# Performance work log

Hardware: AMD Instinct MI355X
Metric: run time of the kernel (lower is better)

Reference implementation:

```python
import jax, jax.numpy as jnp
import numpy as np

HID = 256
HEADS = 8
HD = HID // HEADS  # head_dim = 32


def setup_inputs() -> dict:
    key = jax.random.key(0)
    ks = jax.random.split(key, 16)
    B, N = 4, 2048
    s = 0.02
    inp = {
        'x': jax.random.normal(ks[0], (B, N, 4, HID), dtype=jnp.float32),
        'Wq': jax.random.normal(ks[1], (HID, HID), dtype=jnp.float32) * s,
        'bq': jnp.zeros((HID,), jnp.float32),
        'Wk': jax.random.normal(ks[2], (HID, HID), dtype=jnp.float32) * s,
        'bk': jnp.zeros((HID,), jnp.float32),
        'Wv': jax.random.normal(ks[3], (HID, HID), dtype=jnp.float32) * s,
        'bv': jnp.zeros((HID,), jnp.float32),
        'Wvec': jax.random.normal(ks[4], (2 * HID, HID), dtype=jnp.float32) * s,
        'Wo': jax.random.normal(ks[5], (3 * HID, HID), dtype=jnp.float32) * s,
        'bo': jnp.zeros((3 * HID,), jnp.float32),
        'Wg': jax.random.normal(ks[6], (HID, 2 * HID), dtype=jnp.float32) * s,
        'bg': jnp.zeros((HID,), jnp.float32),
        'alpha_dot': jnp.asarray(1.0, jnp.float32),
        'alpha_norm': jnp.asarray(1.0, jnp.float32),
    }
    return inp


def reference(x, Wq, bq, Wk, bk, Wv, bv, Wvec, Wo, bo, Wg, bg, alpha_dot, alpha_norm):
    B, N, _, H = x.shape
    nh, hd = HEADS, HD
    x_scalar = x[:, :, 0]          # (B,N,H)
    vec = x[:, :, 1:]              # (B,N,3,H)

    def lin(a, W, b=None):
        y = a @ W.T
        return y + b if b is not None else y

    # scalar q/k/v -> (B,heads,N,hd)
    q = lin(x_scalar, Wq, bq).reshape(B, N, nh, hd).transpose(0, 2, 1, 3)
    k = lin(x_scalar, Wk, bk).reshape(B, N, nh, hd).transpose(0, 2, 1, 3)
    v = lin(x_scalar, Wv, bv).reshape(B, N, nh, hd).transpose(0, 2, 1, 3)

    # invariant features from vector channels
    vec_proj = lin(vec, Wvec)                  # (B,N,3,2H)
    vec1, vec2 = vec_proj[..., :H], vec_proj[..., H:]
    vec_dot = jnp.sum(vec1 * vec2, axis=-2)    # (B,N,H)
    vec_norm = jnp.linalg.norm(vec, axis=2)    # (B,N,H)

    # equivariant values: (B,heads,N,3*hd)
    vec_v = vec.reshape(B, N, 3, nh, hd).transpose(0, 3, 1, 2, 4).reshape(B, nh, N, 3 * hd)

    # fused attention: one softmax, aggregate scalar v and vector v together
    scale = 1.0 / np.sqrt(hd).astype(np.float32)
    scores = jnp.einsum('bhqd,bhkd->bhqk', q, k) * scale
    attn = jax.nn.softmax(scores, axis=-1)
    v_all = jnp.concatenate([v, vec_v], axis=-1)        # (B,h,N,4*hd)
    out_all = jnp.einsum('bhqk,bhkd->bhqd', attn, v_all)
    out_s, out_v = out_all[..., :hd], out_all[..., hd:]

    x_out = out_s.transpose(0, 2, 1, 3).reshape(B, N, H)
    vec_aggr = out_v.reshape(B, nh, N, 3, hd).transpose(0, 2, 3, 1, 4).reshape(B, N, 3, H)

    invariants = jnp.concatenate([alpha_dot * vec_dot, alpha_norm * vec_norm], axis=-1)
    gate = jax.nn.sigmoid(lin(invariants, Wg, bg))[:, :, None, :]  # (B,N,1,H)
    vec_combined = gate * vec_aggr + vec  # vector_mixing='add', gating=True

    o = lin(x_out, Wo, bo)
    o1, o2, o3 = o[..., :H], o[..., H:2 * H], o[..., 2 * H:]
    x_updated = vec_dot * o1 + vec_norm * o2 + o3

    x_final = jnp.concatenate([x_updated[:, :, None, :], vec_combined], axis=2)  # (B,N,4,H)
    return x_final
```

## Files before the change

kernel.cpp:

```cpp
#include <hip/hip_runtime.h>
#include <cstdint>
#include <cstddef>

#define HIDN 256
#define NHEAD 8
#define HD 32
#define NSEQ 2048
#define QS (0.17677669529663687f * 1.4426950408889634f)

typedef __attribute__((ext_vector_type(8))) short short8;
typedef __attribute__((ext_vector_type(4))) short short4v;
typedef __attribute__((ext_vector_type(4))) float f32x4;
typedef __attribute__((ext_vector_type(16))) float f32x16;
typedef __attribute__((ext_vector_type(4))) uint32_t u32x4;

static __device__ __forceinline__ short f2bf(float f) {
    union { float f; uint32_t u; } v; v.f = f;
    uint32_t r = (v.u + 0x7FFF + ((v.u >> 16) & 1)) >> 16;
    return (short)r;
}
static __device__ __forceinline__ float bf2f(short s) {
    union { uint32_t u; float f; } v; v.u = ((uint32_t)(uint16_t)s) << 16;
    return v.f;
}

static __device__ __forceinline__ float ex2(float x) {
#if defined(__has_builtin)
#if __has_builtin(__builtin_amdgcn_exp2f)
    return __builtin_amdgcn_exp2f(x);
#else
    return exp2f(x);
#endif
#else
    return exp2f(x);
#endif
}

static __device__ __forceinline__ uint32_t pkbf16(float lo, float hi) {
    uint32_t r;
    asm("v_cvt_pk_bf16_f32 %0, %1, %2" : "=v"(r) : "v"(lo), "v"(hi));
    return r;
}

static __device__ __forceinline__ void half_bcast(uint32_t x, uint32_t& lo, uint32_t& hi) {
    uint32_t a = x, b = x;
    asm("v_permlane32_swap_b32 %0, %1" : "+v"(a), "+v"(b));
    lo = a; hi = b;
}

static __device__ __forceinline__ void gload16(const void* g, void* l) {
    __builtin_amdgcn_global_load_lds(
        (__attribute__((address_space(1))) void*)g,
        (__attribute__((address_space(3))) void*)l, 16, 0, 0);
}

static __device__ __forceinline__ f32x16 zero16() {
    f32x16 z;
    #pragma unroll
    for (int i = 0; i < 16; i++) z[i] = 0.f;
    return z;
}

__global__ __launch_bounds__(256) void wcvt_kernel(
    const float* __restrict__ Wq, const float* __restrict__ Wk,
    const float* __restrict__ Wv, const float* __restrict__ Wvec,
    const float* __restrict__ Wo, const float* __restrict__ Wg,
    const float* __restrict__ bq, const float* __restrict__ bk,
    const float* __restrict__ bv,
    const float* __restrict__ ad, const float* __restrict__ an,
    short* __restrict__ Wqkvb, short* __restrict__ Wvecb,
    short* __restrict__ Wob, short* __restrict__ Wgb, float* __restrict__ bqkvs)
{
    int idx = blockIdx.x * 256 + threadIdx.x;
    if (idx < 65536)        Wqkvb[idx] = f2bf(Wq[idx] * QS);
    else if (idx < 131072)  Wqkvb[idx] = f2bf(Wk[idx - 65536]);
    else if (idx < 196608)  Wqkvb[idx] = f2bf(Wv[idx - 131072]);
    else if (idx < 327680)  Wvecb[idx - 196608] = f2bf(Wvec[idx - 196608]);
    else if (idx < 524288)  Wob[idx - 327680] = f2bf(Wo[idx - 327680]);
    else {
        int i2 = idx - 524288;
        int k = i2 & 511;
        float s = (k < 256) ? ad[0] : an[0];
        Wgb[i2] = f2bf(Wg[i2] * s);
    }
    if (idx < 256)          bqkvs[idx] = bq[idx] * QS;
    else if (idx < 512)     bqkvs[idx] = bk[idx - 256];
    else if (idx < 768)     bqkvs[idx] = bv[idx - 512];
}

__global__ __launch_bounds__(256) void qkv_kernel(
    const float* __restrict__ x, const short* __restrict__ Wqkvb,
    const float* __restrict__ bqkvs,
    short* __restrict__ qbf, short* __restrict__ kbf, short* __restrict__ vtb)
{
    __shared__ short xs[32 * 264];
    __shared__ short vtmp[256 * 34];
    const int tid = threadIdx.x;
    const int m0 = blockIdx.x * 32;
    const int b  = m0 >> 11;
    const int n0 = m0 & 2047;

    #pragma unroll
    for (int l = 0; l < 8; l++) {
        int i = l * 256 + tid;
        int t = i >> 6, j4 = i & 63;
        float4 v = *(const float4*)(x + (size_t)(m0 + t) * 1024 + j4 * 4);
        short4v s = { f2bf(v.x), f2bf(v.y), f2bf(v.z), f2bf(v.w) };
        *(short4v*)&xs[t * 264 + j4 * 4] = s;
    }
    __syncthreads();

    const int wave = tid >> 6, lane = tid & 63;
    const int col = lane & 15, quad = lane >> 4;

    short8 xf[2][8];
    #pragma unroll
    for (int mt = 0; mt < 2; mt++)
        #pragma unroll
        for (int kk = 0; kk < 8; kk++)
            xf[mt][kk] = *(const short8*)&xs[(mt * 16 + col) * 264 + kk * 32 + quad * 8];

    #pragma unroll
    for (int y = 0; y < 3; y++) {
        f32x4 acc[2][4];
        #pragma unroll
        for (int mt = 0; mt < 2; mt++)
            #pragma unroll
            for (int nt = 0; nt < 4; nt++) acc[mt][nt] = (f32x4){0.f,0.f,0.f,0.f};

        const short* Wb = Wqkvb + (size_t)(y * 256 + wave * 64) * 256;
        #pragma unroll
        for (int kk = 0; kk < 8; kk++) {
            #pragma unroll
            for (int nt = 0; nt < 4; nt++) {
                short8 wf = *(const short8*)(Wb + (size_t)(nt * 16 + col) * 256 + kk * 32 + quad * 8);
                #pragma unroll
                for (int mt = 0; mt < 2; mt++)
                    acc[mt][nt] = __builtin_amdgcn_mfma_f32_16x16x32_bf16(wf, xf[mt][kk], acc[mt][nt], 0, 0, 0);
            }
        }

        if (y == 0) {
            #pragma unroll
            for (int nt = 0; nt < 4; nt++) {
                int ch = wave * 64 + nt * 16 + quad * 4;
                float4 bi = *(const float4*)&bqkvs[ch];
                int h = ch >> 5, d = ch & 31;
                #pragma unroll
                for (int mt = 0; mt < 2; mt++) {
                    int n = n0 + mt * 16 + col;
                    short4v s = { f2bf(acc[mt][nt][0] + bi.x), f2bf(acc[mt][nt][1] + bi.y),
                                  f2bf(acc[mt][nt][2] + bi.z), f2bf(acc[mt][nt][3] + bi.w) };
                    *(short4v*)(qbf + ((size_t)(b * 8 + h) * 2048 + n) * 32 + d) = s;
                }
            }
        } else if (y == 1) {
            #pragma unroll
            for (int nt = 0; nt < 4; nt++) {
                int ch = wave * 64 + nt * 16 + quad * 4;
                float4 bi = *(const float4*)&bqkvs[256 + ch];
                int h = ch >> 5, d = ch & 31;
                #pragma unroll
                for (int mt = 0; mt < 2; mt++) {
                    int n = n0 + mt * 16 + col;
                    short4v s = { f2bf(acc[mt][nt][0] + bi.x), f2bf(acc[mt][nt][1] + bi.y),
                                  f2bf(acc[mt][nt][2] + bi.z), f2bf(acc[mt][nt][3] + bi.w) };
                    int f  = ((n & 63) >> 5) * 2 + (d >> 4);
                    int lk = (n & 31) + (((d >> 3) & 1) << 5);
                    short* dst = kbf + ((size_t)(b * 8 + h) * 32 + (n >> 6)) * 2048
                               + f * 512 + lk * 8 + (d & 7);
                    *(short4v*)dst = s;
                }
            }
        } else {
            #pragma unroll
            for (int nt = 0; nt < 4; nt++) {
                int ch = wave * 64 + nt * 16 + quad * 4;
                float4 bi = *(const float4*)&bqkvs[512 + ch];
                #pragma unroll
                for (int mt = 0; mt < 2; mt++) {
                    int tok = mt * 16 + col;
                    vtmp[(ch + 0) * 34 + tok] = f2bf(acc[mt][nt][0] + bi.x);
                    vtmp[(ch + 1) * 34 + tok] = f2bf(acc[mt][nt][1] + bi.y);
                    vtmp[(ch + 2) * 34 + tok] = f2bf(acc[mt][nt][2] + bi.z);
                    vtmp[(ch + 3) * 34 + tok] = f2bf(acc[mt][nt][3] + bi.w);
                }
            }
        }
    }
    __syncthreads();
    {
        int ch = tid;
        short s[32];
        #pragma unroll
        for (int t = 0; t < 32; t++) s[t] = vtmp[ch * 34 + t];
        int h = ch >> 5, d = ch & 31;
        size_t tile = (size_t)(b * 8 + h) * 32 + (n0 >> 6);
        short* dst = vtb + tile * 8192;
        #pragma unroll
        for (int g = 0; g < 4; g++) {
            int kbse = (n0 & 63) + g * 8;
            int f = kbse >> 4;
            int h2 = (kbse >> 3) & 1;
            *(short8*)(dst + f * 512 + (d + h2 * 32) * 8) = *(short8*)&s[g * 8];
        }
    }
}

__global__ __launch_bounds__(512) void vec_kernel(
    const float* __restrict__ x, const short* __restrict__ Wvecb,
    float* __restrict__ dotb, short* __restrict__ invb,
    float* __restrict__ normb, short* __restrict__ vtb)
{
    __shared__ short vb[3 * 16 * 264];
    const int tid = threadIdx.x;
    const int m0 = blockIdx.x * 16;
    const int b = m0 >> 11, n0 = m0 & 2047;

    #pragma unroll
    for (int p = 0; p < 6; p++) {
        int f4 = p * 512 + tid;
        int t = f4 / 192;
        int rem = f4 - t * 192;
        int c = rem >> 6, j4 = rem & 63;
        float4 v = *(const float4*)(x + (size_t)(m0 + t) * 1024 + 256 + c * 256 + j4 * 4);
        short4v s = { f2bf(v.x), f2bf(v.y), f2bf(v.z), f2bf(v.w) };
        *(short4v*)&vb[(c * 16 + t) * 264 + j4 * 4] = s;
    }
    __syncthreads();

    const int wave = tid >> 6, lane = tid & 63;
    const int col = lane & 15, quad = lane >> 4;
    const int j0 = wave * 32;

    f32x4 d1[3][2], d2[3][2];
    #pragma unroll
    for (int c = 0; c < 3; c++)
        #pragma unroll
        for (int nt = 0; nt < 2; nt++) {
            d1[c][nt] = (f32x4){0.f,0.f,0.f,0.f};
            d2[c][nt] = (f32x4){0.f,0.f,0.f,0.f};
        }

    #pragma unroll
    for (int kk = 0; kk < 8; kk++) {
        short8 w1[2], w2[2];
        #pragma unroll
        for (int nt = 0; nt < 2; nt++) {
            w1[nt] = *(const short8*)&Wvecb[(size_t)(j0 + nt * 16 + col) * 256 + kk * 32 + quad * 8];
            w2[nt] = *(const short8*)&Wvecb[(size_t)(256 + j0 + nt * 16 + col) * 256 + kk * 32 + quad * 8];
        }
        #pragma unroll
        for (int c = 0; c < 3; c++) {
            short8 xf = *(const short8*)&vb[(c * 16 + col) * 264 + kk * 32 + quad * 8];
            #pragma unroll
            for (int nt = 0; nt < 2; nt++) {
                d1[c][nt] = __builtin_amdgcn_mfma_f32_16x16x32_bf16(w1[nt], xf, d1[c][nt], 0, 0, 0);
                d2[c][nt] = __builtin_amdgcn_mfma_f32_16x16x32_bf16(w2[nt], xf, d2[c][nt], 0, 0, 0);
            }
        }
    }
    #pragma unroll
    for (int nt = 0; nt < 2; nt++) {
        f32x4 dac = d1[0][nt] * d2[0][nt] + d1[1][nt] * d2[1][nt] + d1[2][nt] * d2[2][nt];
        float4 o = { dac[0], dac[1], dac[2], dac[3] };
        *(float4*)&dotb[(size_t)(m0 + col) * 256 + j0 + nt * 16 + quad * 4] = o;
        short4v s = { f2bf(dac[0]), f2bf(dac[1]), f2bf(dac[2]), f2bf(dac[3]) };
        *(short4v*)&invb[(size_t)(m0 + col) * 512 + j0 + nt * 16 + quad * 4] = s;
    }

    const int j = tid & 255, tp = tid >> 8;
    const int h = j >> 5, d = j & 31;
    #pragma unroll
    for (int t8 = 0; t8 < 8; t8++) {
        int t = tp * 8 + t8;
        float v0 = bf2f(vb[(0 * 16 + t) * 264 + j]);
        float v1 = bf2f(vb[(1 * 16 + t) * 264 + j]);
        float v2 = bf2f(vb[(2 * 16 + t) * 264 + j]);
        float nm = sqrtf(v0 * v0 + v1 * v1 + v2 * v2);
        normb[(size_t)(m0 + t) * 256 + j] = nm;
        invb[(size_t)(m0 + t) * 512 + 256 + j] = f2bf(nm);
    }
    {
        size_t tile = (size_t)(b * 8 + h) * 32 + (n0 >> 6);
        int kbse = (n0 & 63) + tp * 8;
        int ks = kbse >> 4, h2 = (kbse >> 3) & 1;
        #pragma unroll
        for (int c = 0; c < 3; c++) {
            short8 s;
            #pragma unroll
            for (int t8 = 0; t8 < 8; t8++) s[t8] = vb[(c * 16 + tp * 8 + t8) * 264 + j];
            int f = (1 + c) * 4 + ks;
            *(short8*)(vtb + tile * 8192 + f * 512 + (d + h2 * 32) * 8) = s;
        }
    }
}

__global__ __launch_bounds__(512) void attn_kernel(
    const short* __restrict__ qb, const short* __restrict__ kb,
    const short* __restrict__ vtb,
    short* __restrict__ xob, short* __restrict__ ovb)
{
    __shared__ __align__(16) union {
        struct { short Ks[2][2][2048]; short Vs[2][2][8192]; } s;
        struct { float om[4][16][64][4]; float lm[256]; } m;
    } u;
    const int tid = threadIdx.x;
    const int wave = tid >> 6, lane = tid & 63;
    const int g = wave >> 2;
    const int lwave = wave & 3, lt = tid & 255;
    const int q32 = lane & 31, hi = lane >> 5;

    const int D = blockIdx.x;
    const int slot = D >> 3;
    const int bh = (D & 7) + ((slot & 3) << 3);
    const int qt = slot >> 2;
    const int m0 = qt * 128 + lwave * 32;
    const int b = bh >> 3, h = bh & 7;

    const short* qbase = qb + (size_t)bh * NSEQ * HD;
    const short* ksrc  = kb + (size_t)bh * 32 * 2048;
    const short* vsrc  = vtb + (size_t)bh * 32 * 8192;

    short8 qfrag[2];
    #pragma unroll
    for (int ks = 0; ks < 2; ks++)
        qfrag[ks] = *(const short8*)(qbase + (size_t)(m0 + q32) * 32 + ks * 16 + hi * 8);

    f32x16 o[4];
    #pragma unroll
    for (int dt = 0; dt < 4; dt++) o[dt] = zero16();
    float lrun = 0.f;

    auto STAGE = [&](int buf, int t) {
        gload16(ksrc + (size_t)t * 2048 + lt * 8, &u.s.Ks[g][buf][(lt >> 6) * 512]);
        const short* vp = vsrc + (size_t)t * 8192 + lt * 8;
        #pragma unroll
        for (int p = 0; p < 4; p++)
            gload16(vp + p * 2048, &u.s.Vs[g][buf][p * 2048 + (lt >> 6) * 512]);
    };

    STAGE(0, g * 16);
    __syncthreads();

    for (int t = 0; t < 16; t++) {
        const int cur = t & 1;
        if (t < 15) STAGE(cur ^ 1, g * 16 + t + 1);

        short8 kf[4];
        #pragma unroll
        for (int f = 0; f < 4; f++)
            kf[f] = *(const short8*)&u.s.Ks[g][cur][f * 512 + lane * 8];

        #pragma unroll
        for (int tt = 0; tt < 2; tt++) {
            f32x16 a = zero16();
            a = __builtin_amdgcn_mfma_f32_32x32x16_bf16(kf[2*tt+0], qfrag[0], a, 0, 0, 0);
            a = __builtin_amdgcn_mfma_f32_32x32x16_bf16(kf[2*tt+1], qfrag[1], a, 0, 0, 0);

            #pragma unroll
            for (int sx = 0; sx < 2; sx++) {
                float e0 = ex2(a[8*sx+0]), e1 = ex2(a[8*sx+1]);
                float e2 = ex2(a[8*sx+2]), e3 = ex2(a[8*sx+3]);
                float e4 = ex2(a[8*sx+4]), e5 = ex2(a[8*sx+5]);
                float e6 = ex2(a[8*sx+6]), e7 = ex2(a[8*sx+7]);
                lrun += ((e0 + e1) + (e2 + e3)) + ((e4 + e5) + (e6 + e7));
                uint32_t al0, ah0, bl0, bh0, al1, ah1, bl1, bh1;
                half_bcast(pkbf16(e0, e1), al0, ah0);
                half_bcast(pkbf16(e2, e3), bl0, bh0);
                half_bcast(pkbf16(e4, e5), al1, ah1);
                half_bcast(pkbf16(e6, e7), bl1, bh1);
                uint32_t u0 = hi ? al1 : al0;
                uint32_t u1 = hi ? bl1 : bl0;
                uint32_t u2 = hi ? ah1 : ah0;
                uint32_t u3 = hi ? bh1 : bh0;
                u32x4 pv = { u0, u1, u2, u3 };
                short8 pf = __builtin_bit_cast(short8, pv);
                const int s = tt * 2 + sx;
                #pragma unroll
                for (int dt = 0; dt < 4; dt++) {
                    short8 vf = *(const short8*)&u.s.Vs[g][cur][(dt * 4 + s) * 512 + lane * 8];
                    o[dt] = __builtin_amdgcn_mfma_f32_32x32x16_bf16(vf, pf, o[dt], 0, 0, 0);
                }
            }
        }
        __syncthreads();
    }

    float lpart = lrun + __shfl_xor(lrun, 32);

    if (g == 1) {
        #pragma unroll
        for (int dt = 0; dt < 4; dt++)
            #pragma unroll
            for (int q4 = 0; q4 < 4; q4++) {
                f32x4 c = { o[dt][q4*4+0], o[dt][q4*4+1], o[dt][q4*4+2], o[dt][q4*4+3] };
                *(f32x4*)&u.m.om[lwave][dt * 4 + q4][lane][0] = c;
            }
        u.m.lm[lwave * 64 + lane] = lpart;
    }
    __syncthreads();
    if (g == 0) {
        #pragma unroll
        for (int dt = 0; dt < 4; dt++)
            #pragma unroll
            for (int q4 = 0; q4 < 4; q4++) {
                f32x4 c = *(const f32x4*)&u.m.om[lwave][dt * 4 + q4][lane][0];
                o[dt][q4*4+0] += c[0]; o[dt][q4*4+1] += c[1];
                o[dt][q4*4+2] += c[2]; o[dt][q4*4+3] += c[3];
            }
        float l = lpart + u.m.lm[lwave * 64 + lane];
        float linv = 1.0f / l;

        size_t mg = (size_t)b * 2048 + m0 + q32;
        short* xr = xob + mg * 256 + h * 32;
        #pragma unroll
        for (int gg = 0; gg < 4; gg++) {
            short4v sv = { f2bf(o[0][4*gg+0] * linv), f2bf(o[0][4*gg+1] * linv),
                           f2bf(o[0][4*gg+2] * linv), f2bf(o[0][4*gg+3] * linv) };
            *(short4v*)(xr + gg * 8 + hi * 4) = sv;
        }
        short* vr = ovb + mg * 768 + h * 32;
        #pragma unroll
        for (int dt = 1; dt < 4; dt++) {
            #pragma unroll
            for (int gg = 0; gg < 4; gg++) {
                short4v sv = { f2bf(o[dt][4*gg+0] * linv), f2bf(o[dt][4*gg+1] * linv),
                               f2bf(o[dt][4*gg+2] * linv), f2bf(o[dt][4*gg+3] * linv) };
                *(short4v*)(vr + (dt - 1) * 256 + gg * 8 + hi * 4) = sv;
            }
        }
    }
}

__global__ __launch_bounds__(512, 4) void ogemm_kernel(
    const float* __restrict__ x, const short* __restrict__ xob,
    const short* __restrict__ invb,
    const float* __restrict__ dotb, const float* __restrict__ normb,
    const short* __restrict__ ovb,
    const short* __restrict__ Wob, const short* __restrict__ Wgb,
    const float* __restrict__ bo, const float* __restrict__ bg,
    float* __restrict__ out)
{
    __shared__ __align__(16) union {
        struct { short inv[16 * 520]; short xo[16 * 264]; } in;
        struct { short gate[16 * 264]; short o[16 * 776]; } ob;
    } u;
    const int tid = threadIdx.x;
    const int M0 = blockIdx.x * 16;

    #pragma unroll
    for (int l = 0; l < 2; l++) {
        int i = l * 512 + tid;
        int m = i >> 6, seg = i & 63;
        *(short8*)&u.in.inv[m * 520 + seg * 8] =
            *(const short8*)(invb + (size_t)(M0 + m) * 512 + seg * 8);
    }
    {
        int m = tid >> 5, seg = tid & 31;
        *(short8*)&u.in.xo[m * 264 + seg * 8] =
            *(const short8*)(xob + (size_t)(M0 + m) * 256 + seg * 8);
    }
    __syncthreads();

    const int wave = tid >> 6, lane = tid & 63;
    const int col = lane & 15, quad = lane >> 4;
    const int cg = wave * 32;
    const int co = wave * 96;

    f32x4 accg[2], acco[6];
    #pragma unroll
    for (int i = 0; i < 2; i++) accg[i] = (f32x4){0.f,0.f,0.f,0.f};
    #pragma unroll
    for (int i = 0; i < 6; i++) acco[i] = (f32x4){0.f,0.f,0.f,0.f};

    #pragma unroll
    for (int kk = 0; kk < 8; kk++) {
        short8 wg0 = *(const short8*)(Wgb + (size_t)(cg + col) * 512 + (2*kk) * 32 + quad * 8);
        short8 wg1 = *(const short8*)(Wgb + (size_t)(cg + 16 + col) * 512 + (2*kk) * 32 + quad * 8);
        short8 wg2 = *(const short8*)(Wgb + (size_t)(cg + col) * 512 + (2*kk+1) * 32 + quad * 8);
        short8 wg3 = *(const short8*)(Wgb + (size_t)(cg + 16 + col) * 512 + (2*kk+1) * 32 + quad * 8);
        short8 wo0 = *(const short8*)(Wob + (size_t)(co + 0*16 + col) * 256 + kk * 32 + quad * 8);
        short8 wo1 = *(const short8*)(Wob + (size_t)(co + 1*16 + col) * 256 + kk * 32 + quad * 8);
        short8 wo2 = *(const short8*)(Wob + (size_t)(co + 2*16 + col) * 256 + kk * 32 + quad * 8);
        short8 wo3 = *(const short8*)(Wob + (size_t)(co + 3*16 + col) * 256 + kk * 32 + quad * 8);
        short8 wo4 = *(const short8*)(Wob + (size_t)(co + 4*16 + col) * 256 + kk * 32 + quad * 8);
        short8 wo5 = *(const short8*)(Wob + (size_t)(co + 5*16 + col) * 256 + kk * 32 + quad * 8);
        short8 xg0 = *(const short8*)&u.in.inv[col * 520 + (2*kk) * 32 + quad * 8];
        short8 xg1 = *(const short8*)&u.in.inv[col * 520 + (2*kk+1) * 32 + quad * 8];
        short8 xoo = *(const short8*)&u.in.xo[col * 264 + kk * 32 + quad * 8];
        __builtin_amdgcn_sched_barrier(0);
        accg[0] = __builtin_amdgcn_mfma_f32_16x16x32_bf16(wg0, xg0, accg[0], 0, 0, 0);
        accg[1] = __builtin_amdgcn_mfma_f32_16x16x32_bf16(wg1, xg0, accg[1], 0, 0, 0);
        accg[0] = __builtin_amdgcn_mfma_f32_16x16x32_bf16(wg2, xg1, accg[0], 0, 0, 0);
        accg[1] = __builtin_amdgcn_mfma_f32_16x16x32_bf16(wg3, xg1, accg[1], 0, 0, 0);
        acco[0] = __builtin_amdgcn_mfma_f32_16x16x32_bf16(wo0, xoo, acco[0], 0, 0, 0);
        acco[1] = __builtin_amdgcn_mfma_f32_16x16x32_bf16(wo1, xoo, acco[1], 0, 0, 0);
        acco[2] = __builtin_amdgcn_mfma_f32_16x16x32_bf16(wo2, xoo, acco[2], 0, 0, 0);
        acco[3] = __builtin_amdgcn_mfma_f32_16x16x32_bf16(wo3, xoo, acco[3], 0, 0, 0);
        acco[4] = __builtin_amdgcn_mfma_f32_16x16x32_bf16(wo4, xoo, acco[4], 0, 0, 0);
        acco[5] = __builtin_amdgcn_mfma_f32_16x16x32_bf16(wo5, xoo, acco[5], 0, 0, 0);
    }
    __syncthreads();

    #pragma unroll
    for (int i = 0; i < 2; i++) {
        int ch = cg + i * 16 + quad * 4;
        float4 bi = *(const float4*)&bg[ch];
        short4v s = { f2bf(1.f / (1.f + __expf(-(accg[i][0] + bi.x)))),
                      f2bf(1.f / (1.f + __expf(-(accg[i][1] + bi.y)))),
                      f2bf(1.f / (1.f + __expf(-(accg[i][2] + bi.z)))),
                      f2bf(1.f / (1.f + __expf(-(accg[i][3] + bi.w)))) };
        *(short4v*)&u.ob.gate[col * 264 + ch] = s;
    }
    #pragma unroll
    for (int i = 0; i < 6; i++) {
        int ch = co + i * 16 + quad * 4;
        float4 bi = *(const float4*)&bo[ch];
        short4v s = { f2bf(acco[i][0] + bi.x), f2bf(acco[i][1] + bi.y),
                      f2bf(acco[i][2] + bi.z), f2bf(acco[i][3] + bi.w) };
        *(short4v*)&u.ob.o[col * 776 + ch] = s;
    }
    __syncthreads();

    #pragma unroll
    for (int l = 0; l < 8; l++) {
        int idx4 = l * 512 + tid;
        int m = idx4 >> 8;
        int j = (idx4 & 255) * 4;
        size_t mg = (size_t)(M0 + m);
        if (j < 256) {
            float4 dv = *(const float4*)(dotb + mg * 256 + j);
            float4 nv = *(const float4*)(normb + mg * 256 + j);
            short4v o1 = *(short4v*)&u.ob.o[m * 776 + j];
            short4v o2 = *(short4v*)&u.ob.o[m * 776 + 256 + j];
            short4v o3 = *(short4v*)&u.ob.o[m * 776 + 512 + j];
            float4 r;
            r.x = dv.x * bf2f(o1[0]) + nv.x * bf2f(o2[0]) + bf2f(o3[0]);
            r.y = dv.y * bf2f(o1[1]) + nv.y * bf2f(o2[1]) + bf2f(o3[1]);
            r.z = dv.z * bf2f(o1[2]) + nv.z * bf2f(o2[2]) + bf2f(o3[2]);
            r.w = dv.w * bf2f(o1[3]) + nv.w * bf2f(o2[3]) + bf2f(o3[3]);
            *(float4*)(out + mg * 1024 + j) = r;
        } else {
            int c = (j >> 8) - 1, jj = j & 255;
            short4v g4 = *(short4v*)&u.ob.gate[m * 264 + jj];
            short4v av4 = *(const short4v*)(ovb + mg * 768 + c * 256 + jj);
            float4 xv = *(const float4*)(x + mg * 1024 + 256 + c * 256 + jj);
            float4 r = { bf2f(g4[0]) * bf2f(av4[0]) + xv.x, bf2f(g4[1]) * bf2f(av4[1]) + xv.y,
                         bf2f(g4[2]) * bf2f(av4[2]) + xv.z, bf2f(g4[3]) * bf2f(av4[3]) + xv.w };
            *(float4*)(out + mg * 1024 + j) = r;
        }
    }
}

extern "C" void kernel_launch(void* const* d_in, const int* in_sizes, int n_in,
                              void* d_out, int out_size, void* d_ws, size_t ws_size,
                              hipStream_t stream)
{
    const float* x    = (const float*)d_in[0];
    const float* Wq   = (const float*)d_in[1];
    const float* bq   = (const float*)d_in[2];
    const float* Wk   = (const float*)d_in[3];
    const float* bk   = (const float*)d_in[4];
    const float* Wv   = (const float*)d_in[5];
    const float* bv   = (const float*)d_in[6];
    const float* Wvec = (const float*)d_in[7];
    const float* Wo   = (const float*)d_in[8];
    const float* bo   = (const float*)d_in[9];
    const float* Wg   = (const float*)d_in[10];
    const float* bg   = (const float*)d_in[11];
    const float* adp  = (const float*)d_in[12];
    const float* anp  = (const float*)d_in[13];
    float* out = (float*)d_out;

    float* ws    = (float*)d_ws;
    short* qbf   = (short*)ws;
    short* kbf   = (short*)(ws + 1048576);
    short* vtb   = (short*)(ws + 2097152);
    float* dotb  = ws + 6291456;
    float* normb = ws + 8388608;
    short* xob   = (short*)(ws + 10485760);
    short* ovb   = (short*)(ws + 11534336);
    short* invb  = (short*)(ws + 17825792);
    short* Wqkvb = (short*)(ws + 19922944);
    float* bqkvs = ws + 20021248;
    short* Wvecb = (short*)(ws + 20022016);
    short* Wob   = (short*)(ws + 20087552);
    short* Wgb   = (short*)(ws + 20185856);

    wcvt_kernel<<<2560, 256, 0, stream>>>(Wq, Wk, Wv, Wvec, Wo, Wg, bq, bk, bv,
                                          adp, anp, Wqkvb, Wvecb, Wob, Wgb, bqkvs);
    qkv_kernel<<<256, 256, 0, stream>>>(x, Wqkvb, bqkvs, qbf, kbf, vtb);
    vec_kernel<<<512, 512, 0, stream>>>(x, Wvecb, dotb, invb, normb, vtb);
    attn_kernel<<<512, 512, 0, stream>>>(qbf, kbf, vtb, xob, ovb);
    ogemm_kernel<<<512, 512, 0, stream>>>(x, xob, invb, dotb, normb, ovb,
                                          Wob, Wgb, bo, bg, out);
}
```

Measured before the change: 253.5 us.

## Read K fragments from global directly and split merge to shrink LDS

The attention kernel no longer stages K tiles in shared memory. Each wave loads its K fragments straight from global memory, and only V is double-buffered in LDS. The cross-group output merge now runs in two halves through a buffer half the size, with an extra barrier, so the union shrinks to about 64KB and more blocks can be resident per CU. The cost is an uncached-in-LDS global read of K on the critical path of every iteration and two extra synchronisations in the epilogue.

```diff
diff --git a/kernel.cpp b/kernel.cpp
--- a/kernel.cpp
+++ b/kernel.cpp
@@ -302,8 +302,8 @@
     short* __restrict__ xob, short* __restrict__ ovb)
 {
     __shared__ __align__(16) union {
-        struct { short Ks[2][2][2048]; short Vs[2][2][8192]; } s;
-        struct { float om[4][16][64][4]; float lm[256]; } m;
+        short Vs[2][2][8192];
+        struct { float om[4][8][64][4]; float lm[256]; } m;
     } u;
     const int tid = threadIdx.x;
     const int wave = tid >> 6, lane = tid & 63;
@@ -332,25 +332,26 @@
     for (int dt = 0; dt < 4; dt++) o[dt] = zero16();
     float lrun = 0.f;
 
-    auto STAGE = [&](int buf, int t) {
-        gload16(ksrc + (size_t)t * 2048 + lt * 8, &u.s.Ks[g][buf][(lt >> 6) * 512]);
+    auto STAGEV = [&](int buf, int t) {
         const short* vp = vsrc + (size_t)t * 8192 + lt * 8;
         #pragma unroll
         for (int p = 0; p < 4; p++)
-            gload16(vp + p * 2048, &u.s.Vs[g][buf][p * 2048 + (lt >> 6) * 512]);
+            gload16(vp + p * 2048, &u.Vs[g][buf][p * 2048 + (lt >> 6) * 512]);
     };
 
-    STAGE(0, g * 16);
+    STAGEV(0, g * 16);
     __syncthreads();
 
     for (int t = 0; t < 16; t++) {
         const int cur = t & 1;
-        if (t < 15) STAGE(cur ^ 1, g * 16 + t + 1);
+        const int kt = g * 16 + t;
 
         short8 kf[4];
         #pragma unroll
         for (int f = 0; f < 4; f++)
-            kf[f] = *(const short8*)&u.s.Ks[g][cur][f * 512 + lane * 8];
+            kf[f] = *(const short8*)(ksrc + (size_t)kt * 2048 + f * 512 + lane * 8);
+
+        if (t < 15) STAGEV(cur ^ 1, kt + 1);
 
         #pragma unroll
         for (int tt = 0; tt < 2; tt++) {
@@ -379,7 +380,7 @@
                 const int s = tt * 2 + sx;
                 #pragma unroll
                 for (int dt = 0; dt < 4; dt++) {
-                    short8 vf = *(const short8*)&u.s.Vs[g][cur][(dt * 4 + s) * 512 + lane * 8];
+                    short8 vf = *(const short8*)&u.Vs[g][cur][(dt * 4 + s) * 512 + lane * 8];
                     o[dt] = __builtin_amdgcn_mfma_f32_32x32x16_bf16(vf, pf, o[dt], 0, 0, 0);
                 }
             }
@@ -388,10 +389,12 @@
     }
 
     float lpart = lrun + __shfl_xor(lrun, 32);
+    float linv = 0.f;
+    size_t mg = (size_t)b * 2048 + m0 + q32;
 
     if (g == 1) {
         #pragma unroll
-        for (int dt = 0; dt < 4; dt++)
+        for (int dt = 0; dt < 2; dt++)
             #pragma unroll
             for (int q4 = 0; q4 < 4; q4++) {
                 f32x4 c = { o[dt][q4*4+0], o[dt][q4*4+1], o[dt][q4*4+2], o[dt][q4*4+3] };
@@ -402,7 +405,7 @@
     __syncthreads();
     if (g == 0) {
         #pragma unroll
-        for (int dt = 0; dt < 4; dt++)
+        for (int dt = 0; dt < 2; dt++)
             #pragma unroll
             for (int q4 = 0; q4 < 4; q4++) {
                 f32x4 c = *(const f32x4*)&u.m.om[lwave][dt * 4 + q4][lane][0];
@@ -410,9 +413,8 @@
                 o[dt][q4*4+2] += c[2]; o[dt][q4*4+3] += c[3];
             }
         float l = lpart + u.m.lm[lwave * 64 + lane];
-        float linv = 1.0f / l;
-
-        size_t mg = (size_t)b * 2048 + m0 + q32;
+        linv = 1.0f / l;
+
         short* xr = xob + mg * 256 + h * 32;
         #pragma unroll
         for (int gg = 0; gg < 4; gg++) {
@@ -422,7 +424,33 @@
         }
         short* vr = ovb + mg * 768 + h * 32;
         #pragma unroll
-        for (int dt = 1; dt < 4; dt++) {
+        for (int gg = 0; gg < 4; gg++) {
+            short4v sv = { f2bf(o[1][4*gg+0] * linv), f2bf(o[1][4*gg+1] * linv),
+                           f2bf(o[1][4*gg+2] * linv), f2bf(o[1][4*gg+3] * linv) };
+            *(short4v*)(vr + gg * 8 + hi * 4) = sv;
+        }
+    }
+    __syncthreads();
+    if (g == 1) {
+        #pragma unroll
+        for (int dt = 2; dt < 4; dt++)
+            #pragma unroll
+            for (int q4 = 0; q4 < 4; q4++) {
+                f32x4 c = { o[dt][q4*4+0], o[dt][q4*4+1], o[dt][q4*4+2], o[dt][q4*4+3] };
+                *(f32x4*)&u.m.om[lwave][(dt - 2) * 4 + q4][lane][0] = c;
+            }
+    }
+    __syncthreads();
+    if (g == 0) {
+        short* vr = ovb + mg * 768 + h * 32;
+        #pragma unroll
+        for (int dt = 2; dt < 4; dt++) {
+            #pragma unroll
+            for (int q4 = 0; q4 < 4; q4++) {
+                f32x4 c = *(const f32x4*)&u.m.om[lwave][(dt - 2) * 4 + q4][lane][0];
+                o[dt][q4*4+0] += c[0]; o[dt][q4*4+1] += c[1];
+                o[dt][q4*4+2] += c[2]; o[dt][q4*4+3] += c[3];
+            }
             #pragma unroll
             for (int gg = 0; gg < 4; gg++) {
                 short4v sv = { f2bf(o[dt][4*gg+0] * linv), f2bf(o[dt][4*gg+1] * linv),
```

After: 247.2 us. 2.5% less time.
